# Kernel optimization log

Hardware: AMD Instinct MI355X
Metric: run time of the kernel (lower is better)

The kernel has to match this reference:

```python
import jax, jax.numpy as jnp
import numpy as np

B, SQ, SK, D, DV = 2, 1024, 1024, 64, 64
NEG = -1e9


def setup_inputs() -> dict:
    key = jax.random.key(0)
    kq, kk, kv, km = jax.random.split(key, 4)
    return {
        "q": jax.random.normal(kq, (B, SQ, D), dtype=jnp.float32),
        "k": jax.random.normal(kk, (B, SK, D), dtype=jnp.float32),
        "v": jax.random.normal(kv, (B, SK, DV), dtype=jnp.float32),
        "mask": jax.random.randint(km, (B, SK), 0, 2, dtype=jnp.int32),
    }


def reference(q, k, v, mask):
    # L1 (Manhattan) distance scores: [B, Sq, Sk]
    dist = jnp.sum(jnp.abs(q[:, :, None, :] - k[:, None, :, :]), axis=-1)
    scores = -dist
    # mask: [B, Sk] -> broadcast over queries as [B, 1, Sk]
    scores = jnp.where(mask[:, None, :] == 0, NEG, scores)
    attention = jax.nn.softmax(scores, axis=-1)
    # weighted sum of values: [B, Sq, Dv]
    return jnp.einsum("bqk,bkd->bqd", attention, v)
```

## Files before the change

kernel.cpp:

```cpp
#include <hip/hip_runtime.h>
#include <math.h>

#define B_ 2
#define SQ_ 1024
#define SK_ 1024
#define D_ 64
#define DV_ 64
#define QB 4
#define QSCALE 2048.0f
#define QINV (1.0f / 2048.0f)
#define EBIAS 60.0f


__device__ inline unsigned int pk2(float x, float y) {
  int xi = (int)rintf(fminf(fmaxf(x, -15.9f), 15.9f) * QSCALE) + 32768;
  int yi = (int)rintf(fminf(fmaxf(y, -15.9f), 15.9f) * QSCALE) + 32768;
  return (unsigned int)(xi & 0xffff) | ((unsigned int)yi << 16);
}

__global__ __launch_bounds__(256) void convert_qk(const float* __restrict__ qg,
                                                  const float* __restrict__ kg,
                                                  unsigned int* __restrict__ w) {
  const int t = blockIdx.x * 256 + threadIdx.x;
  const float4* s4 = (t < 16384) ? (const float4*)qg : (const float4*)kg;
  const int idx = (t < 16384) ? t : (t - 16384);
  float4 a = s4[idx * 2], b = s4[idx * 2 + 1];
  uint4 r;
  r.x = pk2(a.x, a.y);
  r.y = pk2(a.z, a.w);
  r.z = pk2(b.x, b.y);
  r.w = pk2(b.z, b.w);
  ((uint4*)w)[t] = r;
}

__global__ __launch_bounds__(512, 4) void manh_main(
    const unsigned int* __restrict__ wsq, const unsigned int* __restrict__ wsk,
    const float* __restrict__ vg, const int* __restrict__ maskg,
    float* __restrict__ outg) {
  __shared__ float4 pbuf[SK_];
  __shared__ float4 pvw[8][QB][16];
  __shared__ float4 lw[8];

  const int tid = threadIdx.x;
  const int lane = tid & 63;
  const int wid = tid >> 6;
  const int b = blockIdx.x >> 8;
  const int q0 = (blockIdx.x & 255) * QB;
  const int quarter = lane & 3;
  const int kid = lane >> 2;
  const int kbase = wid * 128;

  const uint4* qrow = (const uint4*)(wsq + ((size_t)b * SQ_ + q0) * 32);
  uint4 qr[QB][2];
#pragma unroll
  for (int q = 0; q < QB; ++q)
#pragma unroll
    for (int j = 0; j < 2; ++j) qr[q][j] = qrow[q * 8 + quarter * 2 + j];

  const uint4* krow = (const uint4*)(wsk + (size_t)b * SK_ * 32);
  const int* mb = maskg + (size_t)b * SK_;

  float lsum[QB] = {0.f, 0.f, 0.f, 0.f};
#pragma unroll
  for (int p = 0; p < 8; ++p) {
    const int key = kbase + p * 16 + kid;
    uint4 ks[2];
#pragma unroll
    for (int j = 0; j < 2; ++j) ks[j] = krow[(size_t)key * 8 + quarter * 2 + j];
    unsigned int d[QB] = {0u, 0u, 0u, 0u};
#pragma unroll
    for (int j = 0; j < 2; ++j) {
#pragma unroll
      for (int q = 0; q < QB; ++q) {
        d[q] = __builtin_amdgcn_sad_u16(qr[q][j].x, ks[j].x, d[q]);
        d[q] = __builtin_amdgcn_sad_u16(qr[q][j].y, ks[j].y, d[q]);
        d[q] = __builtin_amdgcn_sad_u16(qr[q][j].z, ks[j].z, d[q]);
        d[q] = __builtin_amdgcn_sad_u16(qr[q][j].w, ks[j].w, d[q]);
      }
    }
#pragma unroll
    for (int q = 0; q < QB; ++q) {
      d[q] += __shfl_xor(d[q], 1, 64);
      d[q] += __shfl_xor(d[q], 2, 64);
    }
    if (quarter == (p & 3)) {
      const int mk = mb[key];
      float4 pe;
      pe.x = mk ? __expf(fmaf(-(float)d[0], QINV, EBIAS)) : 0.f;
      pe.y = mk ? __expf(fmaf(-(float)d[1], QINV, EBIAS)) : 0.f;
      pe.z = mk ? __expf(fmaf(-(float)d[2], QINV, EBIAS)) : 0.f;
      pe.w = mk ? __expf(fmaf(-(float)d[3], QINV, EBIAS)) : 0.f;
      lsum[0] += pe.x;
      lsum[1] += pe.y;
      lsum[2] += pe.z;
      lsum[3] += pe.w;
      pbuf[key] = pe;
    }
  }
#pragma unroll
  for (int off = 32; off > 0; off >>= 1)
#pragma unroll
    for (int q = 0; q < QB; ++q) lsum[q] += __shfl_down(lsum[q], off, 64);
  if (lane == 0) lw[wid] = make_float4(lsum[0], lsum[1], lsum[2], lsum[3]);

  const int col = lane & 15;
  const int g = lane >> 4;
  const float4* vb4 = (const float4*)(vg + (size_t)b * SK_ * DV_);
  float4 acc[QB];
#pragma unroll
  for (int q = 0; q < QB; ++q) acc[q] = make_float4(0.f, 0.f, 0.f, 0.f);
#pragma unroll 4
  for (int t = 0; t < 32; ++t) {
    const int key = kbase + 4 * t + g;
    float4 v4 = vb4[(size_t)key * 16 + col];
    float4 pw = pbuf[key];
    acc[0].x += pw.x * v4.x; acc[0].y += pw.x * v4.y;
    acc[0].z += pw.x * v4.z; acc[0].w += pw.x * v4.w;
    acc[1].x += pw.y * v4.x; acc[1].y += pw.y * v4.y;
    acc[1].z += pw.y * v4.z; acc[1].w += pw.y * v4.w;
    acc[2].x += pw.z * v4.x; acc[2].y += pw.z * v4.y;
    acc[2].z += pw.z * v4.z; acc[2].w += pw.z * v4.w;
    acc[3].x += pw.w * v4.x; acc[3].y += pw.w * v4.y;
    acc[3].z += pw.w * v4.z; acc[3].w += pw.w * v4.w;
  }
#pragma unroll
  for (int q = 0; q < QB; ++q) {
    acc[q].x += __shfl_xor(acc[q].x, 16, 64);
    acc[q].y += __shfl_xor(acc[q].y, 16, 64);
    acc[q].z += __shfl_xor(acc[q].z, 16, 64);
    acc[q].w += __shfl_xor(acc[q].w, 16, 64);
    acc[q].x += __shfl_xor(acc[q].x, 32, 64);
    acc[q].y += __shfl_xor(acc[q].y, 32, 64);
    acc[q].z += __shfl_xor(acc[q].z, 32, 64);
    acc[q].w += __shfl_xor(acc[q].w, 32, 64);
  }
  if (lane < 16) {
#pragma unroll
    for (int q = 0; q < QB; ++q) pvw[wid][q][col] = acc[q];
  }
  __syncthreads();

  if (tid < 256) {
    const int q2 = tid >> 6;
    const int d2 = tid & 63;
    const float* pf = (const float*)pvw;
    float s = 0.f;
#pragma unroll
    for (int w = 0; w < 8; ++w) s += pf[(w * QB + q2) * 64 + d2];
    float l = 0.f;
#pragma unroll
    for (int w = 0; w < 8; ++w) l += ((const float*)lw)[w * 4 + q2];
    outg[((size_t)b * SQ_ + q0 + q2) * DV_ + d2] = s / l;
  }
}

extern "C" void kernel_launch(void* const* d_in, const int* in_sizes, int n_in,
                              void* d_out, int out_size, void* d_ws,
                              size_t ws_size, hipStream_t stream) {
  const float* q = (const float*)d_in[0];
  const float* k = (const float*)d_in[1];
  const float* v = (const float*)d_in[2];
  const int* mask = (const int*)d_in[3];
  float* out = (float*)d_out;

  unsigned int* wsq = (unsigned int*)d_ws;
  unsigned int* wsk = wsq + 65536;

  convert_qk<<<dim3(128), dim3(256), 0, stream>>>(q, k, wsq);
  manh_main<<<dim3(B_ * (SQ_ / QB)), dim3(512), 0, stream>>>(wsq, wsk, v, mask,
                                                             out);
}
```

Measured before the change: 73.03 us.

## Process eight queries per block with 1024 threads and reuse the LDS buffer

Doubles the number of queries handled per block from four to eight and doubles the block to 16 waves, each covering 64 keys. Every K and V load is now reused across twice as many queries. Exponentials are deferred until after the distance loop, so each lane evaluates its own key once from saved distances. The probability buffer is reused for the per-wave partial outputs, which is safe because each wave reads and writes only its own region. The cost is higher register pressure (8 accumulators and 16 packed query vectors per lane) and only 256 blocks, which may hurt occupancy or cause spills.

```diff
diff --git a/kernel.cpp b/kernel.cpp
--- a/kernel.cpp
+++ b/kernel.cpp
@@ -6,7 +6,7 @@
 #define SK_ 1024
 #define D_ 64
 #define DV_ 64
-#define QB 4
+#define QB 8
 #define QSCALE 2048.0f
 #define QINV (1.0f / 2048.0f)
 #define EBIAS 60.0f
@@ -33,22 +33,21 @@
   ((uint4*)w)[t] = r;
 }
 
-__global__ __launch_bounds__(512, 4) void manh_main(
+__global__ __launch_bounds__(1024, 4) void manh_main(
     const unsigned int* __restrict__ wsq, const unsigned int* __restrict__ wsk,
     const float* __restrict__ vg, const int* __restrict__ maskg,
     float* __restrict__ outg) {
-  __shared__ float4 pbuf[SK_];
-  __shared__ float4 pvw[8][QB][16];
-  __shared__ float4 lw[8];
+  __shared__ float4 pb4[SK_ * 2];
+  __shared__ float lw[16][QB];
 
   const int tid = threadIdx.x;
   const int lane = tid & 63;
   const int wid = tid >> 6;
-  const int b = blockIdx.x >> 8;
-  const int q0 = (blockIdx.x & 255) * QB;
+  const int b = blockIdx.x >> 7;
+  const int q0 = (blockIdx.x & 127) * QB;
   const int quarter = lane & 3;
   const int kid = lane >> 2;
-  const int kbase = wid * 128;
+  const int kbase = wid * 64;
 
   const uint4* qrow = (const uint4*)(wsq + ((size_t)b * SQ_ + q0) * 32);
   uint4 qr[QB][2];
@@ -60,14 +59,16 @@
   const uint4* krow = (const uint4*)(wsk + (size_t)b * SK_ * 32);
   const int* mb = maskg + (size_t)b * SK_;
 
-  float lsum[QB] = {0.f, 0.f, 0.f, 0.f};
+  unsigned int dsave[QB];
 #pragma unroll
-  for (int p = 0; p < 8; ++p) {
+  for (int p = 0; p < 4; ++p) {
     const int key = kbase + p * 16 + kid;
     uint4 ks[2];
 #pragma unroll
     for (int j = 0; j < 2; ++j) ks[j] = krow[(size_t)key * 8 + quarter * 2 + j];
-    unsigned int d[QB] = {0u, 0u, 0u, 0u};
+    unsigned int d[QB];
+#pragma unroll
+    for (int q = 0; q < QB; ++q) d[q] = 0u;
 #pragma unroll
     for (int j = 0; j < 2; ++j) {
 #pragma unroll
@@ -82,26 +83,27 @@
     for (int q = 0; q < QB; ++q) {
       d[q] += __shfl_xor(d[q], 1, 64);
       d[q] += __shfl_xor(d[q], 2, 64);
-    }
-    if (quarter == (p & 3)) {
-      const int mk = mb[key];
-      float4 pe;
-      pe.x = mk ? __expf(fmaf(-(float)d[0], QINV, EBIAS)) : 0.f;
-      pe.y = mk ? __expf(fmaf(-(float)d[1], QINV, EBIAS)) : 0.f;
-      pe.z = mk ? __expf(fmaf(-(float)d[2], QINV, EBIAS)) : 0.f;
-      pe.w = mk ? __expf(fmaf(-(float)d[3], QINV, EBIAS)) : 0.f;
-      lsum[0] += pe.x;
-      lsum[1] += pe.y;
-      lsum[2] += pe.z;
-      lsum[3] += pe.w;
-      pbuf[key] = pe;
+      dsave[q] = (quarter == p) ? d[q] : dsave[q];
     }
   }
+
+  const int okey = kbase + quarter * 16 + kid;
+  const int mk = mb[okey];
+  float pe[QB];
+#pragma unroll
+  for (int q = 0; q < QB; ++q)
+    pe[q] = mk ? __expf(fmaf(-(float)dsave[q], QINV, EBIAS)) : 0.f;
+  pb4[okey * 2 + 0] = make_float4(pe[0], pe[1], pe[2], pe[3]);
+  pb4[okey * 2 + 1] = make_float4(pe[4], pe[5], pe[6], pe[7]);
+
 #pragma unroll
   for (int off = 32; off > 0; off >>= 1)
 #pragma unroll
-    for (int q = 0; q < QB; ++q) lsum[q] += __shfl_down(lsum[q], off, 64);
-  if (lane == 0) lw[wid] = make_float4(lsum[0], lsum[1], lsum[2], lsum[3]);
+    for (int q = 0; q < QB; ++q) pe[q] += __shfl_down(pe[q], off, 64);
+  if (lane == 0) {
+#pragma unroll
+    for (int q = 0; q < QB; ++q) lw[wid][q] = pe[q];
+  }
 
   const int col = lane & 15;
   const int g = lane >> 4;
@@ -110,18 +112,27 @@
 #pragma unroll
   for (int q = 0; q < QB; ++q) acc[q] = make_float4(0.f, 0.f, 0.f, 0.f);
 #pragma unroll 4
-  for (int t = 0; t < 32; ++t) {
+  for (int t = 0; t < 16; ++t) {
     const int key = kbase + 4 * t + g;
     float4 v4 = vb4[(size_t)key * 16 + col];
-    float4 pw = pbuf[key];
-    acc[0].x += pw.x * v4.x; acc[0].y += pw.x * v4.y;
-    acc[0].z += pw.x * v4.z; acc[0].w += pw.x * v4.w;
-    acc[1].x += pw.y * v4.x; acc[1].y += pw.y * v4.y;
-    acc[1].z += pw.y * v4.z; acc[1].w += pw.y * v4.w;
-    acc[2].x += pw.z * v4.x; acc[2].y += pw.z * v4.y;
-    acc[2].z += pw.z * v4.z; acc[2].w += pw.z * v4.w;
-    acc[3].x += pw.w * v4.x; acc[3].y += pw.w * v4.y;
-    acc[3].z += pw.w * v4.z; acc[3].w += pw.w * v4.w;
+    float4 p0 = pb4[key * 2 + 0];
+    float4 p1 = pb4[key * 2 + 1];
+    acc[0].x += p0.x * v4.x; acc[0].y += p0.x * v4.y;
+    acc[0].z += p0.x * v4.z; acc[0].w += p0.x * v4.w;
+    acc[1].x += p0.y * v4.x; acc[1].y += p0.y * v4.y;
+    acc[1].z += p0.y * v4.z; acc[1].w += p0.y * v4.w;
+    acc[2].x += p0.z * v4.x; acc[2].y += p0.z * v4.y;
+    acc[2].z += p0.z * v4.z; acc[2].w += p0.z * v4.w;
+    acc[3].x += p0.w * v4.x; acc[3].y += p0.w * v4.y;
+    acc[3].z += p0.w * v4.z; acc[3].w += p0.w * v4.w;
+    acc[4].x += p1.x * v4.x; acc[4].y += p1.x * v4.y;
+    acc[4].z += p1.x * v4.z; acc[4].w += p1.x * v4.w;
+    acc[5].x += p1.y * v4.x; acc[5].y += p1.y * v4.y;
+    acc[5].z += p1.y * v4.z; acc[5].w += p1.y * v4.w;
+    acc[6].x += p1.z * v4.x; acc[6].y += p1.z * v4.y;
+    acc[6].z += p1.z * v4.z; acc[6].w += p1.z * v4.w;
+    acc[7].x += p1.w * v4.x; acc[7].y += p1.w * v4.y;
+    acc[7].z += p1.w * v4.z; acc[7].w += p1.w * v4.w;
   }
 #pragma unroll
   for (int q = 0; q < QB; ++q) {
@@ -136,20 +147,20 @@
   }
   if (lane < 16) {
 #pragma unroll
-    for (int q = 0; q < QB; ++q) pvw[wid][q][col] = acc[q];
+    for (int q = 0; q < QB; ++q) pb4[wid * 128 + q * 16 + col] = acc[q];
   }
   __syncthreads();
 
-  if (tid < 256) {
+  if (tid < 512) {
     const int q2 = tid >> 6;
     const int d2 = tid & 63;
-    const float* pf = (const float*)pvw;
+    const float* pf = (const float*)pb4;
     float s = 0.f;
 #pragma unroll
-    for (int w = 0; w < 8; ++w) s += pf[(w * QB + q2) * 64 + d2];
+    for (int w = 0; w < 16; ++w) s += pf[w * 512 + q2 * 64 + d2];
     float l = 0.f;
 #pragma unroll
-    for (int w = 0; w < 8; ++w) l += ((const float*)lw)[w * 4 + q2];
+    for (int w = 0; w < 16; ++w) l += lw[w][q2];
     outg[((size_t)b * SQ_ + q0 + q2) * DV_ + d2] = s / l;
   }
 }
@@ -167,6 +178,6 @@
   unsigned int* wsk = wsq + 65536;
 
   convert_qk<<<dim3(128), dim3(256), 0, stream>>>(q, k, wsq);
-  manh_main<<<dim3(B_ * (SQ_ / QB)), dim3(512), 0, stream>>>(wsq, wsk, v, mask,
-                                                             out);
+  manh_main<<<dim3(B_ * (SQ_ / QB)), dim3(1024), 0, stream>>>(wsq, wsk, v,
+                                                              mask, out);
 }
```

Result: slower. 75.92 us (+4.0%).
